# Kernel tuning notes

Measured on AMD Instinct MI355X. Metric: run time of the kernel, lower is better.

The kernel has to match this reference:

```python
import jax, jax.numpy as jnp
import numpy as np
from jax import lax


def setup_inputs() -> dict:
    key = jax.random.key(0)
    ks = jax.random.split(key, 5)
    D, S, T, B, H = 2, 48, 48, 32, 256
    std = 1.0 / np.sqrt(H)
    return {
        "src_input_seq": jax.random.normal(ks[0], (S, B, H), jnp.float32),
        "trg_input_seq": jax.random.normal(ks[1], (T, B, H), jnp.float32),
        "W": jax.random.uniform(ks[2], (D, H, H), jnp.float32, -std, std),
        "U": jax.random.uniform(ks[3], (D, 2 * H, H), jnp.float32, -std, std),
        "b": jax.random.uniform(ks[4], (D, 1, H), jnp.float32, -std, std),
    }


def _grid_layer(x, y, Wd, Ud, bd):
    # x, y: [S, T, B, H] per-cell inputs for this depth
    S, T, B, H = x.shape
    Ux, Uy = Ud[:H], Ud[H:]  # state = concat([state_x, state_y]) @ U

    def row_step(prev_row_hx, row_inputs):
        # prev_row_hx: [T, B, H] = h_x of row i-1 (state_x); zeros for i == 0
        x_row, y_row = row_inputs  # [T, B, H]

        def cell_step(left_hx, inp):
            # left_hx: [B, H] = h_x of cell (i, j-1) (state_y); zeros for j == 0
            up_hx, x_t, y_t = inp
            temp = up_hx @ Ux + left_hx @ Uy + bd  # [B, H]
            h_x = jnp.tanh(x_t @ Wd + temp)
            h_y = jnp.tanh(y_t @ Wd + temp)
            return h_x, (h_x, h_y)

        _, (hx_row, hy_row) = lax.scan(
            cell_step, jnp.zeros((B, H), x.dtype), (prev_row_hx, x_row, y_row)
        )
        return hx_row, (hx_row, hy_row)

    _, (HX, HY) = lax.scan(row_step, jnp.zeros((T, B, H), x.dtype), (x, y))
    return jnp.stack([HX, HY], axis=2)  # [S, T, 2, B, H]


def reference(src_input_seq, trg_input_seq, W, U, b):
    S, B, H = src_input_seq.shape
    T = trg_input_seq.shape[0]
    depth = W.shape[0]
    # depth-0 inputs: x_t = src[i] (same for all j), y_t = trg[j] (same for all i)
    xs = jnp.broadcast_to(src_input_seq[:, None], (S, T, B, H))
    ys = jnp.broadcast_to(trg_input_seq[None, :], (S, T, B, H))
    outs = []
    for d in range(depth):
        Hd = _grid_layer(xs, ys, W[d], U[d], b[d])  # [S, T, 2, B, H]
        outs.append(Hd)
        xs, ys = Hd[:, :, 0], Hd[:, :, 1]
    return jnp.stack(outs, axis=0)  # [depth, S, T, 2, B, H]
```

## Files before the change

### kernel.cpp

```cpp
#include <hip/hip_runtime.h>
#include <hip/hip_bf16.h>


typedef short short8 __attribute__((ext_vector_type(8)));
typedef float f32x4 __attribute__((ext_vector_type(4)));

static constexpr size_t UF_OFF    = 0;
static constexpr size_t WF_OFF    = 512u * 1024;
static constexpr size_t SRCW_OFF  = 768u * 1024;
static constexpr size_t TRGW_OFF  = SRCW_OFF + 48u * 32 * 256 * 4;
static constexpr size_t FLAG0_OFF = TRGW_OFF + 48u * 32 * 256 * 4;
static constexpr size_t FLAG1_OFF = FLAG0_OFF + 48u * 48 * 128;

#define MFMA16(a, b, c) __builtin_amdgcn_mfma_f32_16x16x32_bf16(a, b, c, 0, 0, 0)

__device__ __forceinline__ short f2bf(float f) {
  __hip_bfloat16 h = __float2bfloat16(f);
  return __builtin_bit_cast(short, h);
}

__device__ __forceinline__ size_t plane_off(int d, int s, int t, int c) {
  return (size_t)(((d * 48 + s) * 48 + t) * 2 + c) * 8192u;
}

__device__ __forceinline__ int* flagp(char* ws, size_t off, int s, int t) {
  return (int*)(ws + off) + (size_t)(s * 48 + t) * 32;
}

__device__ __forceinline__ void wait_ge(int* p, int v) {
  while (__hip_atomic_load(p, __ATOMIC_RELAXED, __HIP_MEMORY_SCOPE_AGENT) < v)
    __builtin_amdgcn_s_sleep(1);
  asm volatile("" ::: "memory");
}

__device__ __forceinline__ void st_llc(float* p, float v) {
  __hip_atomic_store(p, v, __ATOMIC_RELAXED, __HIP_MEMORY_SCOPE_AGENT);
}

__device__ __forceinline__ float fast_tanh(float x) {
  float e = exp2f(x * 2.88539008f);
  return 1.f - __fdividef(2.f, e + 1.f);
}

__global__ void preswizzle(const float* __restrict__ U,
                           const float* __restrict__ W,
                           char* __restrict__ ws) {
  int gid = blockIdx.x * 256 + threadIdx.x;
  if (gid < 32768) {
    int r = gid >> 11;
    int d = r >> 3, nh = (r >> 2) & 1, w = r & 3;
    int c = gid & 2047;
    int f = c >> 6, lane = c & 63;
    int nt = f >> 4, ks = f & 15;
    int kbase = ks * 32 + (lane >> 4) * 8;
    int n = nh * 128 + w * 32 + nt * 16 + (lane & 15);
    const float* sp = U + (size_t)d * 512 * 256 + n;
    short8 v;
#pragma unroll
    for (int j = 0; j < 8; ++j) v[j] = f2bf(sp[(size_t)(kbase + j) * 256]);
    *(short8*)(ws + UF_OFF + (size_t)gid * 16) = v;
  } else {
    int idx = gid - 32768;
    int r = idx >> 10;
    int d = r >> 3, nh = (r >> 2) & 1, w = r & 3;
    int c = idx & 1023;
    int f = c >> 6, lane = c & 63;
    int nt = f >> 3, ks = f & 7;
    int kbase = ks * 32 + (lane >> 4) * 8;
    int n = nh * 128 + w * 32 + nt * 16 + (lane & 15);
    const float* sp = W + (size_t)d * 256 * 256 + n;
    short8 v;
#pragma unroll
    for (int j = 0; j < 8; ++j) v[j] = f2bf(sp[(size_t)(kbase + j) * 256]);
    *(short8*)(ws + WF_OFF + (size_t)idx * 16) = v;
  }
}

__global__ __launch_bounds__(256, 1) void precompute_xw(
    const float* __restrict__ src, const float* __restrict__ trg,
    const float* __restrict__ bvec, char* __restrict__ ws) {
  __shared__ __align__(16) char lds[32 * 528];
  const int bid = blockIdx.x;
  const int i = bid >> 1, nh = bid & 1;
  const int tid = threadIdx.x;
  const int w = tid >> 6, lane = tid & 63;
  const int alane = lane & 15, q = lane >> 4;

  short8 bw[2][8];
  {
    const char* wb = ws + WF_OFF + (size_t)(nh * 4 + w) * 16384u + (size_t)lane * 16;
#pragma unroll
    for (int nt = 0; nt < 2; ++nt)
#pragma unroll
      for (int ks = 0; ks < 8; ++ks)
        bw[nt][ks] = *(const short8*)(wb + (nt * 8 + ks) * 1024);
  }

  const float* plane = (i < 48) ? src + (size_t)i * 8192 : trg + (size_t)(i - 48) * 8192;
#pragma unroll
  for (int it = 0; it < 4; ++it) {
    int gid = it * 256 + tid;
    int row = gid >> 5, c = gid & 31;
    const float* p = plane + row * 256 + c * 8;
    short8 v;
#pragma unroll
    for (int j = 0; j < 8; ++j) v[j] = f2bf(p[j]);
    *(short8*)(lds + row * 528 + c * 16) = v;
  }
  __syncthreads();

  const f32x4 zf = {0.f, 0.f, 0.f, 0.f};
  f32x4 acc[2][2];
  acc[0][0] = zf; acc[0][1] = zf; acc[1][0] = zf; acc[1][1] = zf;
  const char* ar0 = lds + alane * 528 + q * 16;
  const char* ar1 = lds + (alane + 16) * 528 + q * 16;
#pragma unroll
  for (int ks = 0; ks < 8; ++ks) {
    short8 a0 = *(const short8*)(ar0 + ks * 64);
    short8 a1 = *(const short8*)(ar1 + ks * 64);
#pragma unroll
    for (int nt = 0; nt < 2; ++nt) {
      acc[0][nt] = MFMA16(a0, bw[nt][ks], acc[0][nt]);
      acc[1][nt] = MFMA16(a1, bw[nt][ks], acc[1][nt]);
    }
  }

  const int n0 = nh * 128 + w * 32 + alane;
  float bs[2] = {bvec[n0], bvec[n0 + 16]};
  const int gtid = (nh * 4 + w) * 64 + lane;
  float* dst = (float*)(ws + (i < 48 ? SRCW_OFF : TRGW_OFF)) +
               (size_t)(i < 48 ? i : i - 48) * 8192 + (size_t)gtid * 16;
#pragma unroll
  for (int mt = 0; mt < 2; ++mt)
#pragma unroll
    for (int nt = 0; nt < 2; ++nt) {
      f32x4 v = acc[mt][nt];
      v[0] += bs[nt]; v[1] += bs[nt]; v[2] += bs[nt]; v[3] += bs[nt];
      ((f32x4*)dst)[mt * 2 + nt] = v;
    }
}

__global__ __launch_bounds__(512, 1) void grid_main(
    float* __restrict__ out, const float* __restrict__ bvec,
    char* __restrict__ ws) {
  __shared__ __align__(16) char lds[4 * 32 * 528];
  char* const buf0 = lds;
  char* const buf1 = lds + 32 * 528;
  char* const buf2 = lds + 2 * 32 * 528;
  char* const buf3 = lds + 3 * 32 * 528;

  const int bid = blockIdx.x;
  const int d = bid / 48;
  const int t = bid % 48;
  const int tid = threadIdx.x;
  const int wv = tid >> 6;
  const int nh = wv >> 2, w = wv & 3;
  const int lane = tid & 63;
  const int alane = lane & 15, q = lane >> 4;
  const int n0 = nh * 128 + w * 32 + alane;

  const float* SRCW = (const float*)(ws + SRCW_OFF);
  const float* TRGW = (const float*)(ws + TRGW_OFF);

  short8 bu[2][16];
  {
    const char* ub = ws + UF_OFF + (size_t)((d * 2 + nh) * 4 + w) * 32768u +
                     (size_t)lane * 16;
#pragma unroll
    for (int nt = 0; nt < 2; ++nt)
#pragma unroll
      for (int ks = 0; ks < 16; ++ks)
        bu[nt][ks] = *(const short8*)(ub + (nt * 16 + ks) * 1024);
  }

  for (int z = tid; z < 32 * 528 / 4; z += 512) ((int*)buf0)[z] = 0;
  __syncthreads();

  const char* up0 = buf0 + alane * 528 + q * 16;
  const char* up1 = buf0 + (alane + 16) * 528 + q * 16;
  const char* l0  = buf1 + alane * 528 + q * 16;
  const char* l1  = buf1 + (alane + 16) * 528 + q * 16;
  const char* y0  = buf2 + alane * 528 + q * 16;
  const char* y1  = buf2 + (alane + 16) * 528 + q * 16;
  const char* m0  = buf3 + alane * 528 + q * 16;
  const char* m1  = buf3 + (alane + 16) * 528 + q * 16;
  const f32x4 zf = {0.f, 0.f, 0.f, 0.f};

  if (d == 0) {
    f32x4 pfy[4];
    {
      const f32x4* py = (const f32x4*)(TRGW + (size_t)t * 8192 + (size_t)tid * 16);
      pfy[0] = py[0]; pfy[1] = py[1]; pfy[2] = py[2]; pfy[3] = py[3];
    }
    for (int s = 0; s < 48; ++s) {
      f32x4 accx[2][2], accy[2][2], accT[2][2];
      {
        const f32x4* px = (const f32x4*)(SRCW + (size_t)s * 8192 + (size_t)tid * 16);
        accx[0][0] = px[0]; accx[0][1] = px[1]; accx[1][0] = px[2]; accx[1][1] = px[3];
      }
      accy[0][0] = pfy[0]; accy[0][1] = pfy[1]; accy[1][0] = pfy[2]; accy[1][1] = pfy[3];
      accT[0][0] = zf; accT[0][1] = zf; accT[1][0] = zf; accT[1][1] = zf;

      f32x4 lva[2], lvb[2];
      if (t > 0) {
        wait_ge(flagp(ws, FLAG0_OFF, s, t - 1), 8);
        const float* pl = out + plane_off(0, s, t - 1, 0);
#pragma unroll
        for (int it = 0; it < 2; ++it) {
          int gid = it * 512 + tid;
          int row = gid >> 5, c = gid & 31;
          const float* p = pl + row * 256 + c * 8;
          lva[it] = *(const f32x4*)p;
          lvb[it] = *(const f32x4*)(p + 4);
        }
      }
#pragma unroll
      for (int ks = 0; ks < 8; ++ks) {
        short8 a0 = *(const short8*)(up0 + ks * 64);
        short8 a1 = *(const short8*)(up1 + ks * 64);
        accT[0][0] = MFMA16(a0, bu[0][ks], accT[0][0]);
        accT[0][1] = MFMA16(a0, bu[1][ks], accT[0][1]);
        accT[1][0] = MFMA16(a1, bu[0][ks], accT[1][0]);
        accT[1][1] = MFMA16(a1, bu[1][ks], accT[1][1]);
      }
      if (t > 0) {
#pragma unroll
        for (int it = 0; it < 2; ++it) {
          int gid = it * 512 + tid;
          int row = gid >> 5, c = gid & 31;
          short8 v;
#pragma unroll
          for (int j = 0; j < 4; ++j) {
            v[j] = f2bf(lva[it][j]);
            v[4 + j] = f2bf(lvb[it][j]);
          }
          *(short8*)(buf1 + row * 528 + c * 16) = v;
        }
      }
      __syncthreads();
      if (t > 0) {
#pragma unroll
        for (int ks = 0; ks < 8; ++ks) {
          short8 a0 = *(const short8*)(l0 + ks * 64);
          short8 a1 = *(const short8*)(l1 + ks * 64);
          accT[0][0] = MFMA16(a0, bu[0][8 + ks], accT[0][0]);
          accT[0][1] = MFMA16(a0, bu[1][8 + ks], accT[0][1]);
          accT[1][0] = MFMA16(a1, bu[0][8 + ks], accT[1][0]);
          accT[1][1] = MFMA16(a1, bu[1][8 + ks], accT[1][1]);
        }
      }
      float hxv[16];
      {
        float* hxp = out + plane_off(0, s, t, 0);
#pragma unroll
        for (int mt = 0; mt < 2; ++mt)
#pragma unroll
          for (int nt = 0; nt < 2; ++nt)
#pragma unroll
            for (int rr = 0; rr < 4; ++rr) {
              int i = (mt * 2 + nt) * 4 + rr;
              int row = mt * 16 + q * 4 + rr, c = n0 + nt * 16;
              float xv = fast_tanh(accx[mt][nt][rr] + accT[mt][nt][rr]);
              hxv[i] = xv;
              st_llc(&hxp[row * 256 + c], xv);
            }
      }
      asm volatile("s_waitcnt vmcnt(0)" ::: "memory");
      if (lane == 0)
        __hip_atomic_fetch_add(flagp(ws, FLAG0_OFF, s, t), 1,
                               __ATOMIC_RELAXED, __HIP_MEMORY_SCOPE_AGENT);
      {
        float* hyp = out + plane_off(0, s, t, 1);
#pragma unroll
        for (int mt = 0; mt < 2; ++mt)
#pragma unroll
          for (int nt = 0; nt < 2; ++nt)
#pragma unroll
            for (int rr = 0; rr < 4; ++rr) {
              int row = mt * 16 + q * 4 + rr, c = n0 + nt * 16;
              st_llc(&hyp[row * 256 + c],
                     fast_tanh(accy[mt][nt][rr] + accT[mt][nt][rr]));
            }
      }
      asm volatile("s_waitcnt vmcnt(0)" ::: "memory");
      if (lane == 0)
        __hip_atomic_fetch_add(flagp(ws, FLAG0_OFF, s, t) + 1, 1,
                               __ATOMIC_RELAXED, __HIP_MEMORY_SCOPE_AGENT);
#pragma unroll
      for (int mt = 0; mt < 2; ++mt)
#pragma unroll
        for (int nt = 0; nt < 2; ++nt)
#pragma unroll
          for (int rr = 0; rr < 4; ++rr) {
            int row = mt * 16 + q * 4 + rr, c = n0 + nt * 16;
            *(short*)(buf0 + row * 528 + c * 2) = f2bf(hxv[(mt * 2 + nt) * 4 + rr]);
          }
      __syncthreads();
    }
  } else {
    const char* wbp = ws + WF_OFF + (size_t)((2 + nh) * 4 + w) * 16384u +
                      (size_t)lane * 16;
    const float bsa = bvec[256 + n0], bsb = bvec[256 + n0 + 16];
    const f32x4 bA = {bsa, bsa, bsa, bsa};
    const f32x4 bB = {bsb, bsb, bsb, bsb};
    for (int s = 0; s < 48; ++s) {
      f32x4 accx[2][2], accy[2][2], accT[2][2];
      accx[0][0] = bA; accx[0][1] = bB; accx[1][0] = bA; accx[1][1] = bB;
      accy[0][0] = bA; accy[0][1] = bB; accy[1][0] = bA; accy[1][1] = bB;
      accT[0][0] = zf; accT[0][1] = zf; accT[1][0] = zf; accT[1][1] = zf;

      wait_ge(flagp(ws, FLAG0_OFF, s, t) + 1, 8);
      f32x4 xva[4], xvb[4];
      {
        const float* px = out + plane_off(0, s, t, 0);
        const float* py = out + plane_off(0, s, t, 1);
#pragma unroll
        for (int it = 0; it < 4; ++it) {
          int gid = it * 512 + tid;
          int pidx = gid >> 10, row = (gid >> 5) & 31, c = gid & 31;
          const float* pp = (pidx ? py : px) + row * 256 + c * 8;
          xva[it] = *(const f32x4*)pp;
          xvb[it] = *(const f32x4*)(pp + 4);
        }
      }
#pragma unroll
      for (int ks = 0; ks < 8; ++ks) {
        short8 a0 = *(const short8*)(up0 + ks * 64);
        short8 a1 = *(const short8*)(up1 + ks * 64);
        accT[0][0] = MFMA16(a0, bu[0][ks], accT[0][0]);
        accT[0][1] = MFMA16(a0, bu[1][ks], accT[0][1]);
        accT[1][0] = MFMA16(a1, bu[0][ks], accT[1][0]);
        accT[1][1] = MFMA16(a1, bu[1][ks], accT[1][1]);
      }
      {
#pragma unroll
        for (int it = 0; it < 4; ++it) {
          int gid = it * 512 + tid;
          int pidx = gid >> 10, row = (gid >> 5) & 31, c = gid & 31;
          char* db = pidx ? buf2 : buf1;
          short8 v;
#pragma unroll
          for (int j = 0; j < 4; ++j) {
            v[j] = f2bf(xva[it][j]);
            v[4 + j] = f2bf(xvb[it][j]);
          }
          *(short8*)(db + row * 528 + c * 16) = v;
        }
      }
      __syncthreads();
#pragma unroll
      for (int ks = 0; ks < 8; ++ks) {
        short8 b0 = *(const short8*)(wbp + ks * 1024);
        short8 b1 = *(const short8*)(wbp + (8 + ks) * 1024);
        short8 ax0 = *(const short8*)(l0 + ks * 64);
        short8 ax1 = *(const short8*)(l1 + ks * 64);
        short8 ay0 = *(const short8*)(y0 + ks * 64);
        short8 ay1 = *(const short8*)(y1 + ks * 64);
        accx[0][0] = MFMA16(ax0, b0, accx[0][0]);
        accx[0][1] = MFMA16(ax0, b1, accx[0][1]);
        accx[1][0] = MFMA16(ax1, b0, accx[1][0]);
        accx[1][1] = MFMA16(ax1, b1, accx[1][1]);
        accy[0][0] = MFMA16(ay0, b0, accy[0][0]);
        accy[0][1] = MFMA16(ay0, b1, accy[0][1]);
        accy[1][0] = MFMA16(ay1, b0, accy[1][0]);
        accy[1][1] = MFMA16(ay1, b1, accy[1][1]);
      }
      if (t > 0) {
        wait_ge(flagp(ws, FLAG1_OFF, s, t - 1), 8);
        const float* pl = out + plane_off(1, s, t - 1, 0);
        f32x4 lva[2], lvb[2];
#pragma unroll
        for (int it = 0; it < 2; ++it) {
          int gid = it * 512 + tid;
          int row = gid >> 5, c = gid & 31;
          const float* p = pl + row * 256 + c * 8;
          lva[it] = *(const f32x4*)p;
          lvb[it] = *(const f32x4*)(p + 4);
        }
#pragma unroll
        for (int it = 0; it < 2; ++it) {
          int gid = it * 512 + tid;
          int row = gid >> 5, c = gid & 31;
          short8 v;
#pragma unroll
          for (int j = 0; j < 4; ++j) {
            v[j] = f2bf(lva[it][j]);
            v[4 + j] = f2bf(lvb[it][j]);
          }
          *(short8*)(buf3 + row * 528 + c * 16) = v;
        }
      }
      __syncthreads();
      if (t > 0) {
#pragma unroll
        for (int ks = 0; ks < 8; ++ks) {
          short8 a0 = *(const short8*)(m0 + ks * 64);
          short8 a1 = *(const short8*)(m1 + ks * 64);
          accT[0][0] = MFMA16(a0, bu[0][8 + ks], accT[0][0]);
          accT[0][1] = MFMA16(a0, bu[1][8 + ks], accT[0][1]);
          accT[1][0] = MFMA16(a1, bu[0][8 + ks], accT[1][0]);
          accT[1][1] = MFMA16(a1, bu[1][8 + ks], accT[1][1]);
        }
      }
      float hxv[16];
      {
        float* hxp = out + plane_off(1, s, t, 0);
#pragma unroll
        for (int mt = 0; mt < 2; ++mt)
#pragma unroll
          for (int nt = 0; nt < 2; ++nt)
#pragma unroll
            for (int rr = 0; rr < 4; ++rr) {
              int i = (mt * 2 + nt) * 4 + rr;
              int row = mt * 16 + q * 4 + rr, c = n0 + nt * 16;
              float xv = fast_tanh(accx[mt][nt][rr] + accT[mt][nt][rr]);
              hxv[i] = xv;
              st_llc(&hxp[row * 256 + c], xv);
            }
      }
      asm volatile("s_waitcnt vmcnt(0)" ::: "memory");
      if (lane == 0)
        __hip_atomic_fetch_add(flagp(ws, FLAG1_OFF, s, t), 1,
                               __ATOMIC_RELAXED, __HIP_MEMORY_SCOPE_AGENT);
      {
        float* hyp = out + plane_off(1, s, t, 1);
#pragma unroll
        for (int mt = 0; mt < 2; ++mt)
#pragma unroll
          for (int nt = 0; nt < 2; ++nt)
#pragma unroll
            for (int rr = 0; rr < 4; ++rr) {
              int row = mt * 16 + q * 4 + rr, c = n0 + nt * 16;
              hyp[row * 256 + c] =
                  fast_tanh(accy[mt][nt][rr] + accT[mt][nt][rr]);
            }
      }
#pragma unroll
      for (int mt = 0; mt < 2; ++mt)
#pragma unroll
        for (int nt = 0; nt < 2; ++nt)
#pragma unroll
          for (int rr = 0; rr < 4; ++rr) {
            int row = mt * 16 + q * 4 + rr, c = n0 + nt * 16;
            *(short*)(buf0 + row * 528 + c * 2) = f2bf(hxv[(mt * 2 + nt) * 4 + rr]);
          }
      __syncthreads();
    }
  }
}

extern "C" void kernel_launch(void* const* d_in, const int* in_sizes, int n_in,
                              void* d_out, int out_size, void* d_ws, size_t ws_size,
                              hipStream_t stream) {
  const float* src = (const float*)d_in[0];
  const float* trg = (const float*)d_in[1];
  const float* W   = (const float*)d_in[2];
  const float* U   = (const float*)d_in[3];
  const float* bv  = (const float*)d_in[4];
  float* out = (float*)d_out;
  char* ws = (char*)d_ws;

  hipMemsetAsync(ws + FLAG0_OFF, 0, 2u * 48 * 48 * 128, stream);
  preswizzle<<<192, 256, 0, stream>>>(U, W, ws);
  precompute_xw<<<192, 256, 0, stream>>>(src, trg, bv, ws);
  grid_main<<<96, 512, 0, stream>>>(out, bv, ws);
}
```

Measured before the change: 816.8 us.

## Move up-state matmul and h_y store off the wavefront critical path

Result: no change. 822.9 us (+0.8%).

```diff
diff --git a/kernel.cpp b/kernel.cpp
--- a/kernel.cpp
+++ b/kernel.cpp
@@ -5,12 +5,14 @@
 typedef short short8 __attribute__((ext_vector_type(8)));
 typedef float f32x4 __attribute__((ext_vector_type(4)));
 
-static constexpr size_t UF_OFF    = 0;
-static constexpr size_t WF_OFF    = 512u * 1024;
-static constexpr size_t SRCW_OFF  = 768u * 1024;
-static constexpr size_t TRGW_OFF  = SRCW_OFF + 48u * 32 * 256 * 4;
-static constexpr size_t FLAG0_OFF = TRGW_OFF + 48u * 32 * 256 * 4;
-static constexpr size_t FLAG1_OFF = FLAG0_OFF + 48u * 48 * 128;
+static constexpr size_t UF_OFF     = 0;
+static constexpr size_t WF_OFF     = 512u * 1024;
+static constexpr size_t SRCW_OFF   = 768u * 1024;
+static constexpr size_t TRGW_OFF   = SRCW_OFF + 48u * 32 * 256 * 4;
+static constexpr size_t FLAGA0_OFF = TRGW_OFF + 48u * 32 * 256 * 4;
+static constexpr size_t FLAGB0_OFF = FLAGA0_OFF + 48u * 48 * 128;
+static constexpr size_t FLAGA1_OFF = FLAGB0_OFF + 48u * 48 * 128;
+static constexpr size_t FLAG_BYTES = 3u * 48 * 48 * 128;
 
 #define MFMA16(a, b, c) __builtin_amdgcn_mfma_f32_16x16x32_bf16(a, b, c, 0, 0, 0)
 
@@ -36,6 +38,9 @@
 __device__ __forceinline__ void st_llc(float* p, float v) {
   __hip_atomic_store(p, v, __ATOMIC_RELAXED, __HIP_MEMORY_SCOPE_AGENT);
 }
+__device__ __forceinline__ void st_llc_i(int* p, int v) {
+  __hip_atomic_store(p, v, __ATOMIC_RELAXED, __HIP_MEMORY_SCOPE_AGENT);
+}
 
 __device__ __forceinline__ float fast_tanh(float x) {
   float e = exp2f(x * 2.88539008f);
@@ -46,6 +51,11 @@
                            const float* __restrict__ W,
                            char* __restrict__ ws) {
   int gid = blockIdx.x * 256 + threadIdx.x;
+  {
+    int* fz = (int*)(ws + FLAGA0_OFF);
+    const int total = (int)(FLAG_BYTES / 4);
+    for (int i = gid; i < total; i += 192 * 256) st_llc_i(&fz[i], 0);
+  }
   if (gid < 32768) {
     int r = gid >> 11;
     int d = r >> 3, nh = (r >> 2) & 1, w = r & 3;
@@ -140,9 +150,10 @@
     }
 }
 
-__global__ __launch_bounds__(512, 1) void grid_main(
-    float* __restrict__ out, const float* __restrict__ bvec,
-    char* __restrict__ ws) {
+__global__ __launch_bounds__(512)
+__attribute__((amdgpu_waves_per_eu(1, 2)))
+void grid_main(float* __restrict__ out, const float* __restrict__ bvec,
+               char* __restrict__ ws) {
   __shared__ __align__(16) char lds[4 * 32 * 528];
   char* const buf0 = lds;
   char* const buf1 = lds + 32 * 528;
@@ -161,20 +172,17 @@
 
   const float* SRCW = (const float*)(ws + SRCW_OFF);
   const float* TRGW = (const float*)(ws + TRGW_OFF);
-
-  short8 bu[2][16];
-  {
-    const char* ub = ws + UF_OFF + (size_t)((d * 2 + nh) * 4 + w) * 32768u +
-                     (size_t)lane * 16;
-#pragma unroll
-    for (int nt = 0; nt < 2; ++nt)
-#pragma unroll
-      for (int ks = 0; ks < 16; ++ks)
-        bu[nt][ks] = *(const short8*)(ub + (nt * 16 + ks) * 1024);
-  }
-
-  for (int z = tid; z < 32 * 528 / 4; z += 512) ((int*)buf0)[z] = 0;
-  __syncthreads();
+  const char* ubp = ws + UF_OFF + (size_t)((d * 2 + nh) * 4 + w) * 32768u +
+                    (size_t)lane * 16;
+
+  short8 buL[2][8];
+#pragma unroll
+  for (int nt = 0; nt < 2; ++nt)
+#pragma unroll
+    for (int ks = 0; ks < 8; ++ks) {
+      buL[nt][ks] = *(const short8*)(ubp + (nt * 16 + 8 + ks) * 1024);
+      asm volatile("" : "+v"(buL[nt][ks]));
+    }
 
   const char* up0 = buf0 + alane * 528 + q * 16;
   const char* up1 = buf0 + (alane + 16) * 528 + q * 16;
@@ -186,6 +194,10 @@
   const char* m1  = buf3 + (alane + 16) * 528 + q * 16;
   const f32x4 zf = {0.f, 0.f, 0.f, 0.f};
 
+  f32x4 accTup[2][2];
+  accTup[0][0] = zf; accTup[0][1] = zf; accTup[1][0] = zf; accTup[1][1] = zf;
+  float hyin[16];
+
   if (d == 0) {
     f32x4 pfy[4];
     {
@@ -193,18 +205,31 @@
       pfy[0] = py[0]; pfy[1] = py[1]; pfy[2] = py[2]; pfy[3] = py[3];
     }
     for (int s = 0; s < 48; ++s) {
-      f32x4 accx[2][2], accy[2][2], accT[2][2];
+      if (s > 0) {
+        float* hyp = out + plane_off(0, s - 1, t, 1);
+#pragma unroll
+        for (int mt = 0; mt < 2; ++mt)
+#pragma unroll
+          for (int nt = 0; nt < 2; ++nt)
+#pragma unroll
+            for (int rr = 0; rr < 4; ++rr) {
+              int row = mt * 16 + q * 4 + rr, c = n0 + nt * 16;
+              st_llc(&hyp[row * 256 + c], fast_tanh(hyin[(mt * 2 + nt) * 4 + rr]));
+            }
+        asm volatile("s_waitcnt vmcnt(0)" ::: "memory");
+        if (lane == 0)
+          __hip_atomic_fetch_add(flagp(ws, FLAGB0_OFF, s - 1, t), 1,
+                                 __ATOMIC_RELAXED, __HIP_MEMORY_SCOPE_AGENT);
+      }
+      f32x4 sxv[4];
       {
         const f32x4* px = (const f32x4*)(SRCW + (size_t)s * 8192 + (size_t)tid * 16);
-        accx[0][0] = px[0]; accx[0][1] = px[1]; accx[1][0] = px[2]; accx[1][1] = px[3];
-      }
-      accy[0][0] = pfy[0]; accy[0][1] = pfy[1]; accy[1][0] = pfy[2]; accy[1][1] = pfy[3];
-      accT[0][0] = zf; accT[0][1] = zf; accT[1][0] = zf; accT[1][1] = zf;
-
-      f32x4 lva[2], lvb[2];
+        sxv[0] = px[0]; sxv[1] = px[1]; sxv[2] = px[2]; sxv[3] = px[3];
+      }
       if (t > 0) {
-        wait_ge(flagp(ws, FLAG0_OFF, s, t - 1), 8);
+        wait_ge(flagp(ws, FLAGA0_OFF, s, t - 1), 8);
         const float* pl = out + plane_off(0, s, t - 1, 0);
+        f32x4 lva[2], lvb[2];
 #pragma unroll
         for (int it = 0; it < 2; ++it) {
           int gid = it * 512 + tid;
@@ -213,17 +238,6 @@
           lva[it] = *(const f32x4*)p;
           lvb[it] = *(const f32x4*)(p + 4);
         }
-      }
-#pragma unroll
-      for (int ks = 0; ks < 8; ++ks) {
-        short8 a0 = *(const short8*)(up0 + ks * 64);
-        short8 a1 = *(const short8*)(up1 + ks * 64);
-        accT[0][0] = MFMA16(a0, bu[0][ks], accT[0][0]);
-        accT[0][1] = MFMA16(a0, bu[1][ks], accT[0][1]);
-        accT[1][0] = MFMA16(a1, bu[0][ks], accT[1][0]);
-        accT[1][1] = MFMA16(a1, bu[1][ks], accT[1][1]);
-      }
-      if (t > 0) {
 #pragma unroll
         for (int it = 0; it < 2; ++it) {
           int gid = it * 512 + tid;
@@ -238,15 +252,18 @@
         }
       }
       __syncthreads();
+      f32x4 accT[2][2];
+      accT[0][0] = accTup[0][0]; accT[0][1] = accTup[0][1];
+      accT[1][0] = accTup[1][0]; accT[1][1] = accTup[1][1];
       if (t > 0) {
 #pragma unroll
         for (int ks = 0; ks < 8; ++ks) {
           short8 a0 = *(const short8*)(l0 + ks * 64);
           short8 a1 = *(const short8*)(l1 + ks * 64);
-          accT[0][0] = MFMA16(a0, bu[0][8 + ks], accT[0][0]);
-          accT[0][1] = MFMA16(a0, bu[1][8 + ks], accT[0][1]);
-          accT[1][0] = MFMA16(a1, bu[0][8 + ks], accT[1][0]);
-          accT[1][1] = MFMA16(a1, bu[1][8 + ks], accT[1][1]);
+          accT[0][0] = MFMA16(a0, buL[0][ks], accT[0][0]);
+          accT[0][1] = MFMA16(a0, buL[1][ks], accT[0][1]);
+          accT[1][0] = MFMA16(a1, buL[0][ks], accT[1][0]);
+          accT[1][1] = MFMA16(a1, buL[1][ks], accT[1][1]);
         }
       }
       float hxv[16];
@@ -260,31 +277,16 @@
             for (int rr = 0; rr < 4; ++rr) {
               int i = (mt * 2 + nt) * 4 + rr;
               int row = mt * 16 + q * 4 + rr, c = n0 + nt * 16;
-              float xv = fast_tanh(accx[mt][nt][rr] + accT[mt][nt][rr]);
+              float tv = accT[mt][nt][rr];
+              float xv = fast_tanh(sxv[mt * 2 + nt][rr] + tv);
               hxv[i] = xv;
+              hyin[i] = pfy[mt * 2 + nt][rr] + tv;
               st_llc(&hxp[row * 256 + c], xv);
             }
       }
       asm volatile("s_waitcnt vmcnt(0)" ::: "memory");
       if (lane == 0)
-        __hip_atomic_fetch_add(flagp(ws, FLAG0_OFF, s, t), 1,
-                               __ATOMIC_RELAXED, __HIP_MEMORY_SCOPE_AGENT);
-      {
-        float* hyp = out + plane_off(0, s, t, 1);
-#pragma unroll
-        for (int mt = 0; mt < 2; ++mt)
-#pragma unroll
-          for (int nt = 0; nt < 2; ++nt)
-#pragma unroll
-            for (int rr = 0; rr < 4; ++rr) {
-              int row = mt * 16 + q * 4 + rr, c = n0 + nt * 16;
-              st_llc(&hyp[row * 256 + c],
-                     fast_tanh(accy[mt][nt][rr] + accT[mt][nt][rr]));
-            }
-      }
-      asm volatile("s_waitcnt vmcnt(0)" ::: "memory");
-      if (lane == 0)
-        __hip_atomic_fetch_add(flagp(ws, FLAG0_OFF, s, t) + 1, 1,
+        __hip_atomic_fetch_add(flagp(ws, FLAGA0_OFF, s, t), 1,
                                __ATOMIC_RELAXED, __HIP_MEMORY_SCOPE_AGENT);
 #pragma unroll
       for (int mt = 0; mt < 2; ++mt)
@@ -296,6 +298,36 @@
             *(short*)(buf0 + row * 528 + c * 2) = f2bf(hxv[(mt * 2 + nt) * 4 + rr]);
           }
       __syncthreads();
+      accTup[0][0] = zf; accTup[0][1] = zf; accTup[1][0] = zf; accTup[1][1] = zf;
+      if (s < 47) {
+#pragma unroll
+        for (int ks = 0; ks < 8; ++ks) {
+          short8 b0 = *(const short8*)(ubp + (0 * 16 + ks) * 1024);
+          short8 b1 = *(const short8*)(ubp + (1 * 16 + ks) * 1024);
+          short8 a0 = *(const short8*)(up0 + ks * 64);
+          short8 a1 = *(const short8*)(up1 + ks * 64);
+          accTup[0][0] = MFMA16(a0, b0, accTup[0][0]);
+          accTup[0][1] = MFMA16(a0, b1, accTup[0][1]);
+          accTup[1][0] = MFMA16(a1, b0, accTup[1][0]);
+          accTup[1][1] = MFMA16(a1, b1, accTup[1][1]);
+        }
+      }
+    }
+    {
+      float* hyp = out + plane_off(0, 47, t, 1);
+#pragma unroll
+      for (int mt = 0; mt < 2; ++mt)
+#pragma unroll
+        for (int nt = 0; nt < 2; ++nt)
+#pragma unroll
+          for (int rr = 0; rr < 4; ++rr) {
+            int row = mt * 16 + q * 4 + rr, c = n0 + nt * 16;
+            st_llc(&hyp[row * 256 + c], fast_tanh(hyin[(mt * 2 + nt) * 4 + rr]));
+          }
+      asm volatile("s_waitcnt vmcnt(0)" ::: "memory");
+      if (lane == 0)
+        __hip_atomic_fetch_add(flagp(ws, FLAGB0_OFF, 47, t), 1,
+                               __ATOMIC_RELAXED, __HIP_MEMORY_SCOPE_AGENT);
     }
   } else {
     const char* wbp = ws + WF_OFF + (size_t)((2 + nh) * 4 + w) * 16384u +
@@ -304,16 +336,23 @@
     const f32x4 bA = {bsa, bsa, bsa, bsa};
     const f32x4 bB = {bsb, bsb, bsb, bsb};
     for (int s = 0; s < 48; ++s) {
-      f32x4 accx[2][2], accy[2][2], accT[2][2];
-      accx[0][0] = bA; accx[0][1] = bB; accx[1][0] = bA; accx[1][1] = bB;
-      accy[0][0] = bA; accy[0][1] = bB; accy[1][0] = bA; accy[1][1] = bB;
-      accT[0][0] = zf; accT[0][1] = zf; accT[1][0] = zf; accT[1][1] = zf;
-
-      wait_ge(flagp(ws, FLAG0_OFF, s, t) + 1, 8);
-      f32x4 xva[4], xvb[4];
+      if (s > 0) {
+        float* hyp = out + plane_off(1, s - 1, t, 1);
+#pragma unroll
+        for (int mt = 0; mt < 2; ++mt)
+#pragma unroll
+          for (int nt = 0; nt < 2; ++nt)
+#pragma unroll
+            for (int rr = 0; rr < 4; ++rr) {
+              int row = mt * 16 + q * 4 + rr, c = n0 + nt * 16;
+              hyp[row * 256 + c] = fast_tanh(hyin[(mt * 2 + nt) * 4 + rr]);
+            }
+      }
+      wait_ge(flagp(ws, FLAGB0_OFF, s, t), 8);
       {
         const float* px = out + plane_off(0, s, t, 0);
         const float* py = out + plane_off(0, s, t, 1);
+        f32x4 xva[4], xvb[4];
 #pragma unroll
         for (int it = 0; it < 4; ++it) {
           int gid = it * 512 + tid;
@@ -322,17 +361,6 @@
           xva[it] = *(const f32x4*)pp;
           xvb[it] = *(const f32x4*)(pp + 4);
         }
-      }
-#pragma unroll
-      for (int ks = 0; ks < 8; ++ks) {
-        short8 a0 = *(const short8*)(up0 + ks * 64);
-        short8 a1 = *(const short8*)(up1 + ks * 64);
-        accT[0][0] = MFMA16(a0, bu[0][ks], accT[0][0]);
-        accT[0][1] = MFMA16(a0, bu[1][ks], accT[0][1]);
-        accT[1][0] = MFMA16(a1, bu[0][ks], accT[1][0]);
-        accT[1][1] = MFMA16(a1, bu[1][ks], accT[1][1]);
-      }
-      {
 #pragma unroll
         for (int it = 0; it < 4; ++it) {
           int gid = it * 512 + tid;
@@ -348,6 +376,9 @@
         }
       }
       __syncthreads();
+      f32x4 accx[2][2], accy[2][2];
+      accx[0][0] = bA; accx[0][1] = bB; accx[1][0] = bA; accx[1][1] = bB;
+      accy[0][0] = bA; accy[0][1] = bB; accy[1][0] = bA; accy[1][1] = bB;
 #pragma unroll
       for (int ks = 0; ks < 8; ++ks) {
         short8 b0 = *(const short8*)(wbp + ks * 1024);
@@ -366,7 +397,7 @@
         accy[1][1] = MFMA16(ay1, b1, accy[1][1]);
       }
       if (t > 0) {
-        wait_ge(flagp(ws, FLAG1_OFF, s, t - 1), 8);
+        wait_ge(flagp(ws, FLAGA1_OFF, s, t - 1), 8);
         const float* pl = out + plane_off(1, s, t - 1, 0);
         f32x4 lva[2], lvb[2];
 #pragma unroll
@@ -391,15 +422,18 @@
         }
       }
       __syncthreads();
+      f32x4 accT[2][2];
+      accT[0][0] = accTup[0][0]; accT[0][1] = accTup[0][1];
+      accT[1][0] = accTup[1][0]; accT[1][1] = accTup[1][1];
       if (t > 0) {
 #pragma unroll
         for (int ks = 0; ks < 8; ++ks) {
           short8 a0 = *(const short8*)(m0 + ks * 64);
           short8 a1 = *(const short8*)(m1 + ks * 64);
-          accT[0][0] = MFMA16(a0, bu[0][8 + ks], accT[0][0]);
-          accT[0][1] = MFMA16(a0, bu[1][8 + ks], accT[0][1]);
-          accT[1][0] = MFMA16(a1, bu[0][8 + ks], accT[1][0]);
-          accT[1][1] = MFMA16(a1, bu[1][8 + ks], accT[1][1]);
+          accT[0][0] = MFMA16(a0, buL[0][ks], accT[0][0]);
+          accT[0][1] = MFMA16(a0, buL[1][ks], accT[0][1]);
+          accT[1][0] = MFMA16(a1, buL[0][ks], accT[1][0]);
+          accT[1][1] = MFMA16(a1, buL[1][ks], accT[1][1]);
         }
       }
       float hxv[16];
@@ -413,28 +447,17 @@
             for (int rr = 0; rr < 4; ++rr) {
               int i = (mt * 2 + nt) * 4 + rr;
               int row = mt * 16 + q * 4 + rr, c = n0 + nt * 16;
-              float xv = fast_tanh(accx[mt][nt][rr] + accT[mt][nt][rr]);
+              float tv = accT[mt][nt][rr];
+              float xv = fast_tanh(accx[mt][nt][rr] + tv);
               hxv[i] = xv;
+              hyin[i] = accy[mt][nt][rr] + tv;
               st_llc(&hxp[row * 256 + c], xv);
             }
       }
       asm volatile("s_waitcnt vmcnt(0)" ::: "memory");
       if (lane == 0)
-        __hip_atomic_fetch_add(flagp(ws, FLAG1_OFF, s, t), 1,
+        __hip_atomic_fetch_add(flagp(ws, FLAGA1_OFF, s, t), 1,
                                __ATOMIC_RELAXED, __HIP_MEMORY_SCOPE_AGENT);
-      {
-        float* hyp = out + plane_off(1, s, t, 1);
-#pragma unroll
-        for (int mt = 0; mt < 2; ++mt)
-#pragma unroll
-          for (int nt = 0; nt < 2; ++nt)
-#pragma unroll
-            for (int rr = 0; rr < 4; ++rr) {
-              int row = mt * 16 + q * 4 + rr, c = n0 + nt * 16;
-              hyp[row * 256 + c] =
-                  fast_tanh(accy[mt][nt][rr] + accT[mt][nt][rr]);
-            }
-      }
 #pragma unroll
       for (int mt = 0; mt < 2; ++mt)
 #pragma unroll
@@ -445,6 +468,32 @@
             *(short*)(buf0 + row * 528 + c * 2) = f2bf(hxv[(mt * 2 + nt) * 4 + rr]);
           }
       __syncthreads();
+      accTup[0][0] = zf; accTup[0][1] = zf; accTup[1][0] = zf; accTup[1][1] = zf;
+      if (s < 47) {
+#pragma unroll
+        for (int ks = 0; ks < 8; ++ks) {
+          short8 b0 = *(const short8*)(ubp + (0 * 16 + ks) * 1024);
+          short8 b1 = *(const short8*)(ubp + (1 * 16 + ks) * 1024);
+          short8 a0 = *(const short8*)(up0 + ks * 64);
+          short8 a1 = *(const short8*)(up1 + ks * 64);
+          accTup[0][0] = MFMA16(a0, b0, accTup[0][0]);
+          accTup[0][1] = MFMA16(a0, b1, accTup[0][1]);
+          accTup[1][0] = MFMA16(a1, b0, accTup[1][0]);
+          accTup[1][1] = MFMA16(a1, b1, accTup[1][1]);
+        }
+      }
+    }
+    {
+      float* hyp = out + plane_off(1, 47, t, 1);
+#pragma unroll
+      for (int mt = 0; mt < 2; ++mt)
+#pragma unroll
+        for (int nt = 0; nt < 2; ++nt)
+#pragma unroll
+          for (int rr = 0; rr < 4; ++rr) {
+            int row = mt * 16 + q * 4 + rr, c = n0 + nt * 16;
+            hyp[row * 256 + c] = fast_tanh(hyin[(mt * 2 + nt) * 4 + rr]);
+          }
     }
   }
 }
@@ -460,7 +509,6 @@
   float* out = (float*)d_out;
   char* ws = (char*)d_ws;
 
-  hipMemsetAsync(ws + FLAG0_OFF, 0, 2u * 48 * 48 * 128, stream);
   preswizzle<<<192, 256, 0, stream>>>(U, W, ws);
   precompute_xw<<<192, 256, 0, stream>>>(src, trg, bv, ws);
   grid_main<<<96, 512, 0, stream>>>(out, bv, ws);
```
